# Kernel optimization log

Hardware: AMD Instinct MI355X
Metric: run time of the kernel (lower is better)

The kernel has to match this reference:

```python
import jax, jax.numpy as jnp
import numpy as np

OUTPUT_SIZE = 50000
HIDDEN = 512


def setup_inputs() -> dict:
    key = jax.random.key(0)
    k1, k2, k3, k4 = jax.random.split(key, 4)
    input_value = jax.random.normal(k1, (4, 2048, HIDDEN), dtype=jnp.float32)
    mask_tensor = jax.random.randint(k2, (4, 2048, 32), 0, OUTPUT_SIZE, dtype=jnp.int64)
    weight = jax.random.normal(k3, (OUTPUT_SIZE, HIDDEN), dtype=jnp.float32)
    bias = jax.random.uniform(k4, (OUTPUT_SIZE,), dtype=jnp.float32)
    return {"input_value": input_value, "mask_tensor": mask_tensor,
            "weight": weight, "bias": bias}


def reference(input_value, mask_tensor, weight, bias):
    # gather per-token candidate weights: [b, s, m, h]
    part_weight = weight[mask_tensor]
    # gather per-token candidate biases: [b, s, m]
    part_bias = bias[mask_tensor]
    out = jnp.einsum('bsh,bsmh->bsm', input_value, part_weight) + part_bias
    return jax.nn.relu(out)
```

## Files before the change

kernel.cpp:

```cpp
#include <hip/hip_runtime.h>
#include <hip/hip_bf16.h>

#define HIDDEN 512
#define M_PER_TOKEN 32

__global__ __launch_bounds__(256) void dynamic_ffn_kernel(
    const float* __restrict__ input,
    const int*   __restrict__ mask,
    const float* __restrict__ weight,
    const float* __restrict__ bias,
    float*       __restrict__ out,
    int n_tokens)
{
    const int token = blockIdx.x;
    if (token >= n_tokens) return;

    const int wave = threadIdx.x >> 6;
    const int lane = threadIdx.x & 63;

    const float* in_row = input + (size_t)token * HIDDEN + lane * 8;
    const float4 x0 = *(const float4*)(in_row);
    const float4 x1 = *(const float4*)(in_row + 4);

    const int*  midx = mask + (size_t)token * M_PER_TOKEN + wave * 8;
    float*      orow = out  + (size_t)token * M_PER_TOKEN + wave * 8;

    int idx[8];
#pragma unroll
    for (int j = 0; j < 8; ++j) idx[j] = midx[j];

    float acc[8];
#pragma unroll
    for (int j = 0; j < 8; ++j) {
        const float* w = weight + (size_t)idx[j] * HIDDEN + lane * 8;
        const float4 w0 = *(const float4*)(w);
        const float4 w1 = *(const float4*)(w + 4);
        acc[j] = x0.x * w0.x + x0.y * w0.y + x0.z * w0.z + x0.w * w0.w
               + x1.x * w1.x + x1.y * w1.y + x1.z * w1.z + x1.w * w1.w;
    }

#pragma unroll
    for (int j = 0; j < 8; ++j) {
        float p = acc[j];
#pragma unroll
        for (int off = 32; off > 0; off >>= 1)
            p += __shfl_down(p, off, 64);
        if (lane == 0) {
            float r = p + bias[idx[j]];
            orow[j] = r > 0.0f ? r : 0.0f;
        }
    }
}

extern "C" void kernel_launch(void* const* d_in, const int* in_sizes, int n_in,
                              void* d_out, int out_size, void* d_ws, size_t ws_size,
                              hipStream_t stream) {
    const float* input  = (const float*)d_in[0];
    const int*   mask   = (const int*)  d_in[1];
    const float* weight = (const float*)d_in[2];
    const float* bias   = (const float*)d_in[3];
    float*       out    = (float*)d_out;

    const int n_tokens = in_sizes[0] / HIDDEN;

    dynamic_ffn_kernel<<<n_tokens, 256, 0, stream>>>(
        input, mask, weight, bias, out, n_tokens);
}
```

Before: 215.1 us.

## Stage gathered weight rows via direct global-to-LDS loads and split tokens across two blocks

Weight rows for each token are now loaded with direct global-to-LDS async loads into a 32KB shared buffer, then read back from LDS for the dot products. Each token is split across two blocks of 16 candidate rows, so the grid doubles and each wave handles 4 rows instead of 8. The aim is higher memory-level parallelism and fewer vector registers tied up in gather loads. In exchange it adds a block barrier, LDS traffic and LDS capacity limits on occupancy, and the token bounds check is gone.

```diff
diff --git a/kernel.cpp b/kernel.cpp
--- a/kernel.cpp
+++ b/kernel.cpp
@@ -3,6 +3,11 @@
 
 #define HIDDEN 512
 #define M_PER_TOKEN 32
+#define M_PER_BLOCK 16
+#define ROWS_PER_WAVE 4
+
+typedef __attribute__((address_space(3))) float lds_f;
+typedef const __attribute__((address_space(1))) float glb_f;
 
 __global__ __launch_bounds__(256) void dynamic_ffn_kernel(
     const float* __restrict__ input,
@@ -12,36 +17,45 @@
     float*       __restrict__ out,
     int n_tokens)
 {
-    const int token = blockIdx.x;
-    if (token >= n_tokens) return;
+    __shared__ float lds_w[M_PER_BLOCK][HIDDEN];
 
-    const int wave = threadIdx.x >> 6;
-    const int lane = threadIdx.x & 63;
+    const int token = blockIdx.x >> 1;
+    const int half  = blockIdx.x & 1;
+    const int wave  = threadIdx.x >> 6;
+    const int lane  = threadIdx.x & 63;
+    const int m0    = half * M_PER_BLOCK + wave * ROWS_PER_WAVE;
+    const int r0    = wave * ROWS_PER_WAVE;
+
+    const int* midx = mask + (size_t)token * M_PER_TOKEN + m0;
+    int idx[ROWS_PER_WAVE];
+#pragma unroll
+    for (int j = 0; j < ROWS_PER_WAVE; ++j) idx[j] = midx[j];
+
+#pragma unroll
+    for (int j = 0; j < ROWS_PER_WAVE; ++j) {
+        const float* gsrc = weight + (size_t)idx[j] * HIDDEN + lane * 4;
+#pragma unroll
+        for (int c = 0; c < 2; ++c) {
+            __builtin_amdgcn_global_load_lds(
+                (glb_f*)(gsrc + c * 256),
+                (lds_f*)&lds_w[r0 + j][c * 256],
+                16, 0, 0);
+        }
+    }
 
     const float* in_row = input + (size_t)token * HIDDEN + lane * 8;
     const float4 x0 = *(const float4*)(in_row);
     const float4 x1 = *(const float4*)(in_row + 4);
 
-    const int*  midx = mask + (size_t)token * M_PER_TOKEN + wave * 8;
-    float*      orow = out  + (size_t)token * M_PER_TOKEN + wave * 8;
+    __syncthreads();
 
-    int idx[8];
+    float* orow = out + (size_t)token * M_PER_TOKEN + m0;
 #pragma unroll
-    for (int j = 0; j < 8; ++j) idx[j] = midx[j];
-
-    float acc[8];
-#pragma unroll
-    for (int j = 0; j < 8; ++j) {
-        const float* w = weight + (size_t)idx[j] * HIDDEN + lane * 8;
-        const float4 w0 = *(const float4*)(w);
-        const float4 w1 = *(const float4*)(w + 4);
-        acc[j] = x0.x * w0.x + x0.y * w0.y + x0.z * w0.z + x0.w * w0.w
-               + x1.x * w1.x + x1.y * w1.y + x1.z * w1.z + x1.w * w1.w;
-    }
-
-#pragma unroll
-    for (int j = 0; j < 8; ++j) {
-        float p = acc[j];
+    for (int j = 0; j < ROWS_PER_WAVE; ++j) {
+        const float4 w0 = *(const float4*)&lds_w[r0 + j][lane * 8];
+        const float4 w1 = *(const float4*)&lds_w[r0 + j][lane * 8 + 4];
+        float p = x0.x * w0.x + x0.y * w0.y + x0.z * w0.z + x0.w * w0.w
+                + x1.x * w1.x + x1.y * w1.y + x1.z * w1.z + x1.w * w1.w;
 #pragma unroll
         for (int off = 32; off > 0; off >>= 1)
             p += __shfl_down(p, off, 64);
@@ -63,6 +77,6 @@
 
     const int n_tokens = in_sizes[0] / HIDDEN;
 
-    dynamic_ffn_kernel<<<n_tokens, 256, 0, stream>>>(
+    dynamic_ffn_kernel<<<n_tokens * 2, 256, 0, stream>>>(
         input, mask, weight, bias, out, n_tokens);
 }
```

Result: slower. 219.8 us (+2.2%).

## Convert weight table to fp16 in workspace before gathering rows

Applied to the files above, without the earlier changes.

Adds a pre-pass kernel that converts the whole fp32 weight table to fp16 in the workspace on every call. The gather kernel then reads half-width rows and accumulates in fp32. This halves the bytes of the random row gathers and shrinks the table's cache footprint. In exchange it adds a full read of the table plus a write of the fp16 copy per call, and introduces fp16 rounding of the weights. It falls back to the fp32 path if the workspace is too small.

```diff
diff --git a/kernel.cpp b/kernel.cpp
--- a/kernel.cpp
+++ b/kernel.cpp
@@ -4,12 +4,31 @@
 #define HIDDEN 512
 #define M_PER_TOKEN 32
 
-__global__ __launch_bounds__(256) void dynamic_ffn_kernel(
-    const float* __restrict__ input,
-    const int*   __restrict__ mask,
-    const float* __restrict__ weight,
-    const float* __restrict__ bias,
-    float*       __restrict__ out,
+typedef _Float16 half8 __attribute__((ext_vector_type(8)));
+
+__global__ __launch_bounds__(256) void convert_w_kernel(
+    const float* __restrict__ w,
+    _Float16*    __restrict__ wh,
+    int n_chunks)
+{
+    int i = blockIdx.x * 256 + threadIdx.x;
+    if (i >= n_chunks) return;
+    const float4 a = ((const float4*)w)[2 * i];
+    const float4 b = ((const float4*)w)[2 * i + 1];
+    half8 h;
+    h[0] = (_Float16)a.x; h[1] = (_Float16)a.y;
+    h[2] = (_Float16)a.z; h[3] = (_Float16)a.w;
+    h[4] = (_Float16)b.x; h[5] = (_Float16)b.y;
+    h[6] = (_Float16)b.z; h[7] = (_Float16)b.w;
+    ((half8*)wh)[i] = h;
+}
+
+__global__ __launch_bounds__(256) void dynamic_ffn_f16_kernel(
+    const float*    __restrict__ input,
+    const int*      __restrict__ mask,
+    const _Float16* __restrict__ wh,
+    const float*    __restrict__ bias,
+    float*          __restrict__ out,
     int n_tokens)
 {
     const int token = blockIdx.x;
@@ -22,8 +41,55 @@
     const float4 x0 = *(const float4*)(in_row);
     const float4 x1 = *(const float4*)(in_row + 4);
 
-    const int*  midx = mask + (size_t)token * M_PER_TOKEN + wave * 8;
-    float*      orow = out  + (size_t)token * M_PER_TOKEN + wave * 8;
+    const int* midx = mask + (size_t)token * M_PER_TOKEN + wave * 8;
+    float*     orow = out  + (size_t)token * M_PER_TOKEN + wave * 8;
+
+    int idx[8];
+#pragma unroll
+    for (int j = 0; j < 8; ++j) idx[j] = midx[j];
+
+    float acc[8];
+#pragma unroll
+    for (int j = 0; j < 8; ++j) {
+        const half8 h = *(const half8*)(wh + (size_t)idx[j] * HIDDEN + lane * 8);
+        acc[j] = (float)h[0] * x0.x + (float)h[1] * x0.y
+               + (float)h[2] * x0.z + (float)h[3] * x0.w
+               + (float)h[4] * x1.x + (float)h[5] * x1.y
+               + (float)h[6] * x1.z + (float)h[7] * x1.w;
+    }
+
+#pragma unroll
+    for (int j = 0; j < 8; ++j) {
+        float p = acc[j];
+#pragma unroll
+        for (int off = 32; off > 0; off >>= 1)
+            p += __shfl_down(p, off, 64);
+        if (lane == 0) {
+            float r = p + bias[idx[j]];
+            orow[j] = r > 0.0f ? r : 0.0f;
+        }
+    }
+}
+
+__global__ __launch_bounds__(256) void dynamic_ffn_f32_kernel(
+    const float* __restrict__ input,
+    const int*   __restrict__ mask,
+    const float* __restrict__ weight,
+    const float* __restrict__ bias,
+    float*       __restrict__ out,
+    int n_tokens)
+{
+    const int token = blockIdx.x;
+    if (token >= n_tokens) return;
+    const int wave = threadIdx.x >> 6;
+    const int lane = threadIdx.x & 63;
+
+    const float* in_row = input + (size_t)token * HIDDEN + lane * 8;
+    const float4 x0 = *(const float4*)(in_row);
+    const float4 x1 = *(const float4*)(in_row + 4);
+
+    const int* midx = mask + (size_t)token * M_PER_TOKEN + wave * 8;
+    float*     orow = out  + (size_t)token * M_PER_TOKEN + wave * 8;
 
     int idx[8];
 #pragma unroll
@@ -38,7 +104,6 @@
         acc[j] = x0.x * w0.x + x0.y * w0.y + x0.z * w0.z + x0.w * w0.w
                + x1.x * w1.x + x1.y * w1.y + x1.z * w1.z + x1.w * w1.w;
     }
-
 #pragma unroll
     for (int j = 0; j < 8; ++j) {
         float p = acc[j];
@@ -61,8 +126,19 @@
     const float* bias   = (const float*)d_in[3];
     float*       out    = (float*)d_out;
 
-    const int n_tokens = in_sizes[0] / HIDDEN;
+    const int n_tokens  = in_sizes[0] / HIDDEN;
+    const int w_elems   = in_sizes[2];
+    const size_t need   = (size_t)w_elems * sizeof(_Float16);
 
-    dynamic_ffn_kernel<<<n_tokens, 256, 0, stream>>>(
-        input, mask, weight, bias, out, n_tokens);
+    if (ws_size >= need) {
+        _Float16* wh = (_Float16*)d_ws;
+        const int n_chunks = w_elems / 8;
+        convert_w_kernel<<<(n_chunks + 255) / 256, 256, 0, stream>>>(
+            weight, wh, n_chunks);
+        dynamic_ffn_f16_kernel<<<n_tokens, 256, 0, stream>>>(
+            input, mask, wh, bias, out, n_tokens);
+    } else {
+        dynamic_ffn_f32_kernel<<<n_tokens, 256, 0, stream>>>(
+            input, mask, weight, bias, out, n_tokens);
+    }
 }
```

After: 213.1 us. About the same (-0.9%).
